# Kernel optimization log

Measured on AMD Instinct MI355X. Metric: run time of the kernel, lower is better.

Reference implementation:

```python
import jax, jax.numpy as jnp
from jax import lax
import numpy as np

C = 256
K = 3
PAD = 1


def _bilinear_sample(x, py, px):
    """Zero-padded bilinear sampling.
    x: [B,C,Hin,Win]; py,px: [B,Kt,H,W] float sample coords -> [B,C,Kt,H,W]."""
    B, Cc, Hin, Win = x.shape
    y0 = jnp.floor(py)
    x0 = jnp.floor(px)
    y1 = y0 + 1.0
    x1 = x0 + 1.0
    wy1 = py - y0
    wy0 = 1.0 - wy1
    wx1 = px - x0
    wx0 = 1.0 - wx1
    xf = x.reshape(B, Cc, Hin * Win)

    def corner(yi, xi, wy, wx):
        valid = (yi >= 0) & (yi < Hin) & (xi >= 0) & (xi < Win)
        yc = jnp.clip(yi, 0, Hin - 1).astype(jnp.int32)
        xc = jnp.clip(xi, 0, Win - 1).astype(jnp.int32)
        idx = yc * Win + xc  # [B,Kt,H,W]
        g = jax.vmap(lambda xb, ib: xb[:, ib])(xf, idx)  # [B,C,Kt,H,W]
        w = (wy * wx) * valid.astype(x.dtype)
        return g * w[:, None]

    return (corner(y0, x0, wy0, wx0) + corner(y0, x1, wy0, wx1)
            + corner(y1, x0, wy1, wx0) + corner(y1, x1, wy1, wx1))


def _arm_forward(x, w_off, b_off, w, b):
    B, Cc, H, W = x.shape
    # offset-predicting conv (standard 3x3, pad 1)
    off = lax.conv_general_dilated(
        x, w_off, window_strides=(1, 1), padding=[(PAD, PAD), (PAD, PAD)],
        dimension_numbers=('NCHW', 'OIHW', 'NCHW')) + b_off[None, :, None, None]
    off = off.reshape(B, K * K, 2, H, W)  # [:, k, 0]=dy, [:, k, 1]=dx (mmcv layout)
    ky, kx = jnp.meshgrid(jnp.arange(K), jnp.arange(K), indexing='ij')
    ky = ky.reshape(-1).astype(x.dtype)  # [9]
    kx = kx.reshape(-1).astype(x.dtype)
    base_y = jnp.arange(H, dtype=x.dtype)[None, None, :, None]
    base_x = jnp.arange(W, dtype=x.dtype)[None, None, None, :]
    py = base_y - PAD + ky[None, :, None, None] + off[:, :, 0]  # [B,9,H,W]
    px = base_x - PAD + kx[None, :, None, None] + off[:, :, 1]
    sampled = _bilinear_sample(x, py, px)  # [B,C,9,H,W]
    out = jnp.einsum('bckhw,ock->bohw', sampled, w.reshape(Cc, Cc, K * K))
    out = out + b[None, :, None, None]
    return jax.nn.sigmoid(out)


def setup_inputs() -> dict:
    key = jax.random.key(0)
    k1, k2, k3, k4 = jax.random.split(key, 4)
    B, H, W = 8, 64, 64
    x = jax.random.normal(k1, (B, C, H, W), dtype=jnp.float32)
    # offset conv params (mmcv zero-inits these; use small random to exercise sampling)
    w_off = jax.random.normal(k2, (2 * K * K, C, K, K), dtype=jnp.float32) * 0.01
    b_off = jnp.zeros((2 * K * K,), dtype=jnp.float32)
    # deformable conv weight/bias (kaiming-ish scale)
    scale = 1.0 / np.sqrt(C * K * K)
    w = jax.random.normal(k3, (C, C, K, K), dtype=jnp.float32) * scale
    b = jax.random.normal(k4, (C,), dtype=jnp.float32) * scale
    return {"Fstagei": x, "w_off": w_off, "b_off": b_off, "w": w, "b": b}


def reference(Fstagei, w_off, b_off, w, b):
    return _arm_forward(Fstagei, w_off, b_off, w, b)
```

## Files before the change

### kernel.cpp

```cpp
#include <hip/hip_runtime.h>

typedef unsigned short u16;
typedef unsigned int u32;
typedef __attribute__((ext_vector_type(8))) short short8;
typedef __attribute__((ext_vector_type(4))) float f32x4;

#define BB 8
#define CCH 256
#define HH 64
#define WW 64
#define HP 66
#define NPOS 4096
#define KTOT 2304

#define XT_BYTES   17842176ull
#define W2R_OFF    17842176ull
#define WOFF2_OFF  19021824ull
#define P_OFF      19169280ull
#define OFF2_OFF   40402944ull
#define S_OFF      42762240ull
#define S_BATCH    18874368ull

__device__ __forceinline__ float bf2f(u16 u) {
    union { u32 u; float f; } v; v.u = ((u32)u) << 16; return v.f;
}
__device__ __forceinline__ u16 f2bf(float f) {
    union { float f; u32 u; } v; v.f = f;
    u32 r = v.u + 0x7FFFu + ((v.u >> 16) & 1u);
    return (u16)(r >> 16);
}
__device__ __forceinline__ u32 pk2(float a, float b) {
    return (u32)f2bf(a) | ((u32)f2bf(b) << 16);
}
__device__ __forceinline__ void bf2x2(u32 p, float& a, float& b) {
    union { u32 u; float f; } va, vb;
    va.u = p << 16; vb.u = p & 0xffff0000u;
    a = va.f; b = vb.f;
}
__device__ __forceinline__ void ldg_lds16(const u16* g, u16* l) {
    __builtin_amdgcn_global_load_lds((const __attribute__((address_space(1))) u32*)g,
                                     (__attribute__((address_space(3))) u32*)l, 16, 0, 0);
}

__global__ __launch_bounds__(256) void k_pre(const float* __restrict__ w, const float* __restrict__ w_off,
                                             const float* __restrict__ x,
                                             u16* __restrict__ W2r, u16* __restrict__ Woff2,
                                             u16* __restrict__ xT) {
    __shared__ __align__(16) float SH[4608];
    int bx = blockIdx.x;
    int t = threadIdx.x;
    if (bx < 256) {
        int o = bx;
        const float* src = w + (size_t)o * 2304;
#pragma unroll
        for (int j = 0; j < 9; ++j) SH[j * 256 + t] = src[j * 256 + t];
        __syncthreads();
        u16* dst = W2r + (size_t)o * 2304;
#pragma unroll
        for (int k = 0; k < 9; ++k) dst[k * 256 + t] = f2bf(SH[t * 9 + k]);
    } else if (bx == 256) {
        for (int o2 = 0; o2 < 32; ++o2) {
            if (o2 < 18) {
                const float* src = w_off + (size_t)o2 * 2304;
#pragma unroll
                for (int j = 0; j < 9; ++j) SH[j * 256 + t] = src[j * 256 + t];
                __syncthreads();
#pragma unroll
                for (int k = 0; k < 9; ++k) Woff2[(size_t)o2 * 2304 + k * 256 + t] = f2bf(SH[t * 9 + k]);
                __syncthreads();
            } else {
#pragma unroll
                for (int k = 0; k < 9; ++k) Woff2[(size_t)o2 * 2304 + k * 256 + t] = 0;
            }
        }
    } else if (bx < 777) {
        int idx = (bx - 257) * 4 + (t >> 6);
        int b = idx / 260, m = idx - b * 260;
        int y, xx;
        if (m < 66)       { y = 0;  xx = m; }
        else if (m < 132) { y = 65; xx = m - 66; }
        else if (m < 196) { y = m - 132 + 1; xx = 0; }
        else              { y = m - 196 + 1; xx = 65; }
        u16* p = xT + ((size_t)(b * HP + y) * HP + xx) * CCH + (t & 63) * 4;
        uint2 zz; zz.x = 0; zz.y = 0;
        *(uint2*)p = zz;
    } else {
        int idx = bx - 777;
        int b = idx & 7;
        int r = idx >> 3;
        int y = r & 63, c0 = (r >> 6) * 64;
        {
            int i = t >> 2, seg = t & 3;
            const float* src = x + (((size_t)(b * CCH + c0 + i) * HH + y) * WW) + seg * 16;
            float4 v0 = *(const float4*)(src);
            float4 v1 = *(const float4*)(src + 4);
            float4 v2 = *(const float4*)(src + 8);
            float4 v3 = *(const float4*)(src + 12);
            *(float4*)&SH[i * 72 + seg * 16]      = v0;
            *(float4*)&SH[i * 72 + seg * 16 + 4]  = v1;
            *(float4*)&SH[i * 72 + seg * 16 + 8]  = v2;
            *(float4*)&SH[i * 72 + seg * 16 + 12] = v3;
        }
        __syncthreads();
        {
            int xc = t >> 2, cs = t & 3;
            u16* dst = xT + (((size_t)(b * HP + y + 1) * HP) + (xc + 1)) * CCH + c0 + cs * 16;
            u32 p[8];
#pragma unroll
            for (int j = 0; j < 8; ++j)
                p[j] = pk2(SH[(cs * 16 + 2 * j) * 72 + xc], SH[(cs * 16 + 2 * j + 1) * 72 + xc]);
            uint4 d0, d1;
            d0.x = p[0]; d0.y = p[1]; d0.z = p[2]; d0.w = p[3];
            d1.x = p[4]; d1.y = p[5]; d1.z = p[6]; d1.w = p[7];
            *(uint4*)dst = d0;
            *(uint4*)(dst + 8) = d1;
        }
    }
}

__global__ __launch_bounds__(256) void k_offconv(const u16* __restrict__ xT,
                                                 const u16* __restrict__ Woff2,
                                                 float* __restrict__ P) {
    __shared__ __align__(16) u16 AS[2][2048];
    __shared__ __align__(16) u16 BS[2][8192];
    int b = blockIdx.x, k9 = blockIdx.y;
    int pos0 = blockIdx.z * 128;
    int ky = k9 / 3, kx = k9 % 3;
    int t = threadIdx.x, lane = t & 63, wv = t >> 6;

    int srow = lane >> 3;
    int sw8 = ((lane & 7) ^ srow) << 3;
    const u16* pA = Woff2 + (size_t)k9 * 256;
    const u16* pXb = xT + (size_t)b * HP * HP * CCH;

    f32x4 acc[2][2];
    f32x4 z = {0.f, 0.f, 0.f, 0.f};
    acc[0][0] = z; acc[0][1] = z; acc[1][0] = z; acc[1][1] = z;

    auto stage = [&](int cs, int d) {
        int koff = cs * 64;
        {
            int row = wv * 8 + srow;
            ldg_lds16(pA + (size_t)row * KTOT + koff + sw8, &AS[d][wv * 512]);
        }
#pragma unroll
        for (int i = 0; i < 4; ++i) {
            int inst = wv * 4 + i;
            int rowg = pos0 + inst * 8 + srow;
            int py_ = rowg >> 6, px_ = rowg & 63;
            const u16* g = pXb + (((size_t)(py_ + ky) * HP) + px_ + kx) * CCH + koff + sw8;
            ldg_lds16(g, &BS[d][inst * 512]);
        }
    };

    stage(0, 0);
    __syncthreads();

    int buf = 0;
    int m = lane & 15, q = lane >> 4, key = lane & 7;
    for (int cs = 0; cs < 4; ++cs) {
        if (cs < 3) stage(cs + 1, buf ^ 1);
#pragma unroll
        for (int j = 0; j < 2; ++j) {
            int slot8 = (((j * 4 + q) ^ key) << 3);
            short8 a0 = *(const short8*)&AS[buf][m * 64 + slot8];
            short8 a1 = *(const short8*)&AS[buf][(16 + m) * 64 + slot8];
            short8 b0 = *(const short8*)&BS[buf][(wv * 32 + m) * 64 + slot8];
            short8 b1 = *(const short8*)&BS[buf][(wv * 32 + 16 + m) * 64 + slot8];
            acc[0][0] = __builtin_amdgcn_mfma_f32_16x16x32_bf16(a0, b0, acc[0][0], 0, 0, 0);
            acc[0][1] = __builtin_amdgcn_mfma_f32_16x16x32_bf16(a0, b1, acc[0][1], 0, 0, 0);
            acc[1][0] = __builtin_amdgcn_mfma_f32_16x16x32_bf16(a1, b0, acc[1][0], 0, 0, 0);
            acc[1][1] = __builtin_amdgcn_mfma_f32_16x16x32_bf16(a1, b1, acc[1][1], 0, 0, 0);
        }
        __syncthreads();
        buf ^= 1;
    }
    int nn = lane & 15;
    float* Pp = P + (size_t)(b * 9 + k9) * 18 * NPOS;
#pragma unroll
    for (int ao = 0; ao < 2; ++ao)
#pragma unroll
        for (int bn = 0; bn < 2; ++bn) {
            int pos = pos0 + wv * 32 + bn * 16 + nn;
#pragma unroll
            for (int r = 0; r < 4; ++r) {
                int o = ao * 16 + q * 4 + r;
                if (o < 18) Pp[o * NPOS + pos] = acc[ao][bn][r];
            }
        }
}

__global__ __launch_bounds__(256) void k_reduce(const float* __restrict__ P,
                                                const float* __restrict__ b_off,
                                                float2* __restrict__ off2) {
    int b = blockIdx.x;
    int pos = blockIdx.y * 256 + threadIdx.x;
    float s[18];
#pragma unroll
    for (int o = 0; o < 18; ++o) s[o] = b_off[o];
    const float* Pp = P + (size_t)(b * 9) * 18 * NPOS + pos;
    for (int k9 = 0; k9 < 9; ++k9) {
#pragma unroll
        for (int o = 0; o < 18; ++o)
            s[o] += Pp[(k9 * 18 + o) * NPOS];
    }
#pragma unroll
    for (int op = 0; op < 9; ++op) {
        float2 v; v.x = s[2 * op]; v.y = s[2 * op + 1];
        off2[(((size_t)(b * 9 + op)) << 12) + pos] = v;
    }
}

__global__ __launch_bounds__(256) void k_sample(const u16* __restrict__ xT,
                                                const float2* __restrict__ off2,
                                                u16* __restrict__ S, int b0) {
    int bl = blockIdx.x, b = b0 + bl, k9 = blockIdx.y;
    int pos0 = blockIdx.z * 64;
    int t = threadIdx.x, g = t >> 4, ll = t & 15;
    int ky = k9 / 3, kx = k9 % 3;
    int bbase = b * HP * HP;

    for (int i = 0; i < 4; ++i) {
        int pos = pos0 + g + i * 16;
        int y = pos >> 6, x = pos & 63;
        float2 off = off2[(((size_t)(b * 9 + k9)) << 12) + pos];
        float pyf = (float)(y - 1 + ky) + off.x;
        float pxf = (float)(x - 1 + kx) + off.y;
        float y0f = floorf(pyf), x0f = floorf(pxf);
        int y0 = (int)y0f, x0 = (int)x0f;
        int y1 = y0 + 1, x1 = x0 + 1;
        float wy1 = pyf - y0f, wy0 = 1.f - wy1;
        float wx1 = pxf - x0f, wx0 = 1.f - wx1;
        bool vy0 = (y0 >= 0) & (y0 < HH), vy1 = (y1 >= 0) & (y1 < HH);
        bool vx0 = (x0 >= 0) & (x0 < WW), vx1 = (x1 >= 0) & (x1 < WW);
        int yc0 = min(max(y0, 0), HH - 1), yc1 = min(max(y1, 0), HH - 1);
        int xc0 = min(max(x0, 0), WW - 1), xc1 = min(max(x1, 0), WW - 1);
        float w0 = (vy0 & vx0) ? wy0 * wx0 : 0.f;
        float w1 = (vy0 & vx1) ? wy0 * wx1 : 0.f;
        float w2 = (vy1 & vx0) ? wy1 * wx0 : 0.f;
        float w3 = (vy1 & vx1) ? wy1 * wx1 : 0.f;
        const u16* g0 = xT + (size_t)((bbase + (yc0 + 1) * HP + xc0 + 1)) * CCH;
        const u16* g1 = xT + (size_t)((bbase + (yc0 + 1) * HP + xc1 + 1)) * CCH;
        const u16* g2 = xT + (size_t)((bbase + (yc1 + 1) * HP + xc0 + 1)) * CCH;
        const u16* g3 = xT + (size_t)((bbase + (yc1 + 1) * HP + xc1 + 1)) * CCH;
        u16* sp = S + ((((size_t)(bl * 9 + k9)) << 12) + pos) * CCH;
#pragma unroll
        for (int cp = 0; cp < 2; ++cp) {
            int c = cp * 128 + ll * 8;
            uint4 r0 = *(const uint4*)(g0 + c);
            uint4 r1 = *(const uint4*)(g1 + c);
            uint4 r2 = *(const uint4*)(g2 + c);
            uint4 r3 = *(const uint4*)(g3 + c);
            float v[8];
#pragma unroll
            for (int dw = 0; dw < 4; ++dw) {
                u32 p0 = ((const u32*)&r0)[dw];
                u32 p1 = ((const u32*)&r1)[dw];
                u32 p2 = ((const u32*)&r2)[dw];
                u32 p3 = ((const u32*)&r3)[dw];
                float a0, b0_, a1, b1_, a2, b2_, a3, b3_;
                bf2x2(p0, a0, b0_);
                bf2x2(p1, a1, b1_);
                bf2x2(p2, a2, b2_);
                bf2x2(p3, a3, b3_);
                v[2 * dw]     = w0 * a0 + w1 * a1 + w2 * a2 + w3 * a3;
                v[2 * dw + 1] = w0 * b0_ + w1 * b1_ + w2 * b2_ + w3 * b3_;
            }
            uint4 sv;
            sv.x = pk2(v[0], v[1]); sv.y = pk2(v[2], v[3]);
            sv.z = pk2(v[4], v[5]); sv.w = pk2(v[6], v[7]);
            *(uint4*)(sp + c) = sv;
        }
    }
}

__global__ __launch_bounds__(256) void k_gemm(const u16* __restrict__ S,
                                              const u16* __restrict__ W2r,
                                              const float* __restrict__ bias,
                                              float* __restrict__ out, int b0) {
    __shared__ __align__(16) u16 AS[2][8192];
    __shared__ __align__(16) u16 BS[2][8192];
    int bl = blockIdx.x, b = b0 + bl;
    int o0 = blockIdx.y * 128;
    int pos0 = blockIdx.z * 128;
    int t = threadIdx.x, lane = t & 63, wv = t >> 6;
    int wr = wv >> 1, wc = wv & 1;

    int srow = lane >> 3;
    int sw8 = ((lane & 7) ^ srow) << 3;
    const u16* pA = W2r + (size_t)o0 * KTOT;
    const u16* pSb = S + (((size_t)(bl * 9)) << 12) * CCH;

    f32x4 acc[4][4];
    f32x4 z = {0.f, 0.f, 0.f, 0.f};
#pragma unroll
    for (int i = 0; i < 4; ++i)
#pragma unroll
        for (int j = 0; j < 4; ++j) acc[i][j] = z;

    auto stage = [&](int s, int d) {
        int k9 = s >> 2, cs = s & 3;
        int koffA = k9 * 256 + cs * 64;
        const u16* pB = pSb + ((size_t)k9 << 12) * CCH + cs * 64;
#pragma unroll
        for (int i = 0; i < 4; ++i) {
            int inst = wv * 4 + i;
            int row = inst * 8 + srow;
            ldg_lds16(pA + (size_t)row * KTOT + koffA + sw8, &AS[d][inst * 512]);
            ldg_lds16(pB + (size_t)(pos0 + row) * CCH + sw8, &BS[d][inst * 512]);
        }
    };

    stage(0, 0);
    __syncthreads();

    int buf = 0;
    int m = lane & 15, q = lane >> 4, key = lane & 7;
    for (int step = 0; step < 36; ++step) {
        if (step < 35) stage(step + 1, buf ^ 1);
#pragma unroll
        for (int j = 0; j < 2; ++j) {
            int slot8 = (((j * 4 + q) ^ key) << 3);
            short8 af[4], bfr[4];
#pragma unroll
            for (int ao = 0; ao < 4; ++ao)
                af[ao] = *(const short8*)&AS[buf][(wr * 64 + ao * 16 + m) * 64 + slot8];
#pragma unroll
            for (int bn = 0; bn < 4; ++bn)
                bfr[bn] = *(const short8*)&BS[buf][(wc * 64 + bn * 16 + m) * 64 + slot8];
#pragma unroll
            for (int ao = 0; ao < 4; ++ao)
#pragma unroll
                for (int bn = 0; bn < 4; ++bn)
                    acc[ao][bn] = __builtin_amdgcn_mfma_f32_16x16x32_bf16(af[ao], bfr[bn], acc[ao][bn], 0, 0, 0);
        }
        __syncthreads();
        buf ^= 1;
    }

    int nn = lane & 15;
#pragma unroll
    for (int ao = 0; ao < 4; ++ao) {
        int ob = o0 + wr * 64 + ao * 16 + q * 4;
#pragma unroll
        for (int bn = 0; bn < 4; ++bn) {
            int pos = pos0 + wc * 64 + bn * 16 + nn;
#pragma unroll
            for (int r = 0; r < 4; ++r) {
                float v = acc[ao][bn][r] + bias[ob + r];
                float sg = 1.0f / (1.0f + __expf(-v));
                out[(size_t)((b * CCH + ob + r) * NPOS) + pos] = sg;
            }
        }
    }
}

extern "C" void kernel_launch(void* const* d_in, const int* in_sizes, int n_in,
                              void* d_out, int out_size, void* d_ws, size_t ws_size,
                              hipStream_t stream) {
    const float* x     = (const float*)d_in[0];
    const float* w_off = (const float*)d_in[1];
    const float* b_off = (const float*)d_in[2];
    const float* w     = (const float*)d_in[3];
    const float* bias  = (const float*)d_in[4];
    float* out = (float*)d_out;

    char* ws = (char*)d_ws;
    u16*    xT    = (u16*)ws;
    u16*    W2r   = (u16*)(ws + W2R_OFF);
    u16*    Woff2 = (u16*)(ws + WOFF2_OFF);
    float*  P     = (float*)(ws + P_OFF);
    float2* off2  = (float2*)(ws + OFF2_OFF);
    u16*    S     = (u16*)(ws + S_OFF);

    int nb = 8;
    while (nb > 1 && ws_size < S_OFF + (size_t)nb * S_BATCH) nb >>= 1;
    if (ws_size < S_OFF + S_BATCH) return;

    k_pre<<<2825, 256, 0, stream>>>(w, w_off, x, W2r, Woff2, xT);
    k_offconv<<<dim3(8, 9, 32), 256, 0, stream>>>(xT, Woff2, P);
    k_reduce<<<dim3(8, 16), 256, 0, stream>>>(P, b_off, off2);
    for (int p = 0; p < 8; p += nb) {
        k_sample<<<dim3(nb, 9, 64), 256, 0, stream>>>(xT, off2, S, p);
        k_gemm<<<dim3(nb, 2, 32), 256, 0, stream>>>(S, W2r, bias, out, p);
    }
}
```

Baseline: 209.4 us.

## Widen GEMM block to cover all output channels with finer-grained pipelining

The GEMM now uses 512-thread blocks that each compute all 256 output channels for a 128-position tile. The S tile is therefore loaded once rather than twice across the two former channel-halves. The per-step __syncthreads is replaced with partial vmcnt waits plus raw s_barrier, so the next stage's global-to-LDS loads can stay in flight during compute, and s_setprio raises wave priority around the MFMA burst. This doubles the LDS footprint for A and halves the grid size, which may hurt occupancy and load balance. The barrier and wait-count ordering is delicate: if the vmcnt threshold is wrong, a wave can read a buffer before it is fully written.

```diff
diff --git a/kernel.cpp b/kernel.cpp
--- a/kernel.cpp
+++ b/kernel.cpp
@@ -274,21 +274,20 @@
     }
 }
 
-__global__ __launch_bounds__(256) void k_gemm(const u16* __restrict__ S,
-                                              const u16* __restrict__ W2r,
-                                              const float* __restrict__ bias,
-                                              float* __restrict__ out, int b0) {
-    __shared__ __align__(16) u16 AS[2][8192];
+__global__ __launch_bounds__(512, 2) void k_gemm(const u16* __restrict__ S,
+                                                 const u16* __restrict__ W2r,
+                                                 const float* __restrict__ bias,
+                                                 float* __restrict__ out, int b0) {
+    __shared__ __align__(16) u16 AS[2][16384];
     __shared__ __align__(16) u16 BS[2][8192];
     int bl = blockIdx.x, b = b0 + bl;
-    int o0 = blockIdx.y * 128;
     int pos0 = blockIdx.z * 128;
     int t = threadIdx.x, lane = t & 63, wv = t >> 6;
     int wr = wv >> 1, wc = wv & 1;
 
     int srow = lane >> 3;
     int sw8 = ((lane & 7) ^ srow) << 3;
-    const u16* pA = W2r + (size_t)o0 * KTOT;
+    const u16* pA = W2r;
     const u16* pSb = S + (((size_t)(bl * 9)) << 12) * CCH;
 
     f32x4 acc[4][4];
@@ -307,41 +306,52 @@
             int inst = wv * 4 + i;
             int row = inst * 8 + srow;
             ldg_lds16(pA + (size_t)row * KTOT + koffA + sw8, &AS[d][inst * 512]);
+        }
+#pragma unroll
+        for (int i = 0; i < 2; ++i) {
+            int inst = wv * 2 + i;
+            int row = inst * 8 + srow;
             ldg_lds16(pB + (size_t)(pos0 + row) * CCH + sw8, &BS[d][inst * 512]);
         }
     };
 
     stage(0, 0);
-    __syncthreads();
-
-    int buf = 0;
+
     int m = lane & 15, q = lane >> 4, key = lane & 7;
     for (int step = 0; step < 36; ++step) {
-        if (step < 35) stage(step + 1, buf ^ 1);
+        int cur = step & 1;
+        if (step < 35) {
+            stage(step + 1, cur ^ 1);
+            asm volatile("s_waitcnt vmcnt(6)" ::: "memory");
+        } else {
+            asm volatile("s_waitcnt vmcnt(0)" ::: "memory");
+        }
+        __builtin_amdgcn_s_barrier();
 #pragma unroll
         for (int j = 0; j < 2; ++j) {
             int slot8 = (((j * 4 + q) ^ key) << 3);
             short8 af[4], bfr[4];
 #pragma unroll
             for (int ao = 0; ao < 4; ++ao)
-                af[ao] = *(const short8*)&AS[buf][(wr * 64 + ao * 16 + m) * 64 + slot8];
+                af[ao] = *(const short8*)&AS[cur][(wr * 64 + ao * 16 + m) * 64 + slot8];
 #pragma unroll
             for (int bn = 0; bn < 4; ++bn)
-                bfr[bn] = *(const short8*)&BS[buf][(wc * 64 + bn * 16 + m) * 64 + slot8];
+                bfr[bn] = *(const short8*)&BS[cur][(wc * 64 + bn * 16 + m) * 64 + slot8];
+            __builtin_amdgcn_s_setprio(1);
 #pragma unroll
             for (int ao = 0; ao < 4; ++ao)
 #pragma unroll
                 for (int bn = 0; bn < 4; ++bn)
                     acc[ao][bn] = __builtin_amdgcn_mfma_f32_16x16x32_bf16(af[ao], bfr[bn], acc[ao][bn], 0, 0, 0);
-        }
-        __syncthreads();
-        buf ^= 1;
+            __builtin_amdgcn_s_setprio(0);
+            __builtin_amdgcn_s_barrier();
+        }
     }
 
     int nn = lane & 15;
 #pragma unroll
     for (int ao = 0; ao < 4; ++ao) {
-        int ob = o0 + wr * 64 + ao * 16 + q * 4;
+        int ob = wr * 64 + ao * 16 + q * 4;
 #pragma unroll
         for (int bn = 0; bn < 4; ++bn) {
             int pos = pos0 + wc * 64 + bn * 16 + nn;
@@ -382,6 +392,6 @@
     k_reduce<<<dim3(8, 16), 256, 0, stream>>>(P, b_off, off2);
     for (int p = 0; p < 8; p += nb) {
         k_sample<<<dim3(nb, 9, 64), 256, 0, stream>>>(xT, off2, S, p);
-        k_gemm<<<dim3(nb, 2, 32), 256, 0, stream>>>(S, W2r, bias, out, p);
-    }
-}
+        k_gemm<<<dim3(nb, 1, 32), 512, 0, stream>>>(S, W2r, bias, out, p);
+    }
+}
```

After: 219.3 us. 1.05x slower.
